# Optimization experiments

Measured on AMD Instinct MI355X. Metric: run time of the kernel, lower is better.

The kernel has to match this reference:

```python
import jax, jax.numpy as jnp
import numpy as np

EMBED_DIM = 768
NUM_HEADS = 12
HEAD_DIM = EMBED_DIM // NUM_HEADS
SCALE = HEAD_DIM ** -0.5
EPS = 1e-5


def _layernorm(x, g, b):
    m = jnp.mean(x, axis=-1, keepdims=True)
    v = jnp.mean(jnp.square(x - m), axis=-1, keepdims=True)
    return (x - m) * jax.lax.rsqrt(v + EPS) * g + b


def setup_inputs() -> dict:
    key = jax.random.key(0)
    ks = jax.random.split(key, 8)
    B, N, D, Hd = 16, 1024, EMBED_DIM, HEAD_DIM
    x = jax.random.normal(ks[0], (B, N, D), dtype=jnp.float32)
    W_qkv = jax.random.normal(ks[1], (D, 3 * D), dtype=jnp.float32) * (D ** -0.5)
    b_qkv = jnp.zeros((3 * D,), dtype=jnp.float32)
    W_proj = jax.random.normal(ks[2], (D, D), dtype=jnp.float32) * (D ** -0.5)
    b_proj = jnp.zeros((D,), dtype=jnp.float32)
    return {
        "x": x,
        "ln_g": jnp.ones((D,), jnp.float32), "ln_b": jnp.zeros((D,), jnp.float32),
        "W_qkv": W_qkv, "b_qkv": b_qkv,
        "qn_g": jnp.ones((Hd,), jnp.float32), "qn_b": jnp.zeros((Hd,), jnp.float32),
        "kn_g": jnp.ones((Hd,), jnp.float32), "kn_b": jnp.zeros((Hd,), jnp.float32),
        "W_proj": W_proj, "b_proj": b_proj,
    }


def reference(x, ln_g, ln_b, W_qkv, b_qkv, qn_g, qn_b, kn_g, kn_b, W_proj, b_proj):
    B, N, D = x.shape
    H, Hd = NUM_HEADS, HEAD_DIM
    xn = _layernorm(x, ln_g, ln_b)                      # qkv_norm (pre-LN of embed_dim)
    qkv = xn @ W_qkv + b_qkv                            # [B,N,3D]
    qkv = qkv.reshape(B, N, 3, H, Hd)
    q = jnp.transpose(qkv[:, :, 0], (0, 2, 1, 3))       # [B,H,N,Hd]
    k = jnp.transpose(qkv[:, :, 1], (0, 2, 1, 3))
    v = jnp.transpose(qkv[:, :, 2], (0, 2, 1, 3))
    q = _layernorm(q, qn_g, qn_b)                       # per-head QK LayerNorm
    k = _layernorm(k, kn_g, kn_b)
    attn = jnp.einsum("bhnd,bhmd->bhnm", q, k) * SCALE
    attn = jax.nn.softmax(attn, axis=-1)
    out = jnp.einsum("bhnm,bhmd->bhnd", attn, v)        # [B,H,N,Hd]
    out = jnp.transpose(out, (0, 2, 1, 3)).reshape(B, N, D)
    return out @ W_proj + b_proj
```

## Files before the change

### kernel.cpp

```cpp
#include <hip/hip_runtime.h>

typedef _Float16 half8 __attribute__((ext_vector_type(8)));
typedef _Float16 half4 __attribute__((ext_vector_type(4)));
typedef float f32x4 __attribute__((ext_vector_type(4)));

#define B_    16
#define N_    1024
#define D_    768
#define H_    12
#define M_    (B_ * N_)
#define QKVN_ 2304
#define EPS_  1e-5f
#define QS_   0.18033688011112042f

__device__ __forceinline__ float exp2_fast(float x) {
#if __has_builtin(__builtin_amdgcn_exp2f)
    return __builtin_amdgcn_exp2f(x);
#else
    return __builtin_exp2f(x);
#endif
}

__device__ __forceinline__ void gl16(const _Float16* g, _Float16* l) {
    __builtin_amdgcn_global_load_lds((const __attribute__((address_space(1))) void*)g,
                                     (__attribute__((address_space(3))) void*)l, 16, 0, 0);
}

__global__ __launch_bounds__(256) void convert_w(const float* __restrict__ Wqkv,
                                                 const float* __restrict__ Wproj,
                                                 _Float16* __restrict__ wqkvT,
                                                 _Float16* __restrict__ wprojT) {
    __shared__ float T[64][65];
    int t = blockIdx.x;
    const float* W; _Float16* O; int NW, k0, n0;
    if (t < 432) { W = Wqkv;  O = wqkvT;  NW = QKVN_; k0 = (t % 12) * 64; n0 = (t / 12) * 64; }
    else { t -= 432; W = Wproj; O = wprojT; NW = D_;  k0 = (t % 12) * 64; n0 = (t / 12) * 64; }
    int c = threadIdx.x & 63, r4 = threadIdx.x >> 6;
#pragma unroll
    for (int i = 0; i < 16; ++i) {
        int r = i * 4 + r4;
        T[r][c] = W[(size_t)(k0 + r) * NW + n0 + c];
    }
    __syncthreads();
#pragma unroll
    for (int i = 0; i < 16; ++i) {
        int r = i * 4 + r4;
        O[(size_t)(n0 + r) * D_ + k0 + c] = (_Float16)T[c][r];
    }
}

__global__ __launch_bounds__(256) void ln_embed(const float* __restrict__ x,
                                                const float* __restrict__ g,
                                                const float* __restrict__ bb,
                                                _Float16* __restrict__ xn) {
    int row = blockIdx.x;
    int tid = threadIdx.x;
    const float* xr = x + (size_t)row * D_;
    float v0 = xr[tid], v1 = xr[tid + 256], v2 = xr[tid + 512];
    float s = v0 + v1 + v2;
    float q = v0 * v0 + v1 * v1 + v2 * v2;
#pragma unroll
    for (int m = 32; m >= 1; m >>= 1) {
        s += __shfl_xor(s, m);
        q += __shfl_xor(q, m);
    }
    __shared__ float ss[4], qq[4];
    int wave = tid >> 6;
    if ((tid & 63) == 0) { ss[wave] = s; qq[wave] = q; }
    __syncthreads();
    float S = ss[0] + ss[1] + ss[2] + ss[3];
    float Q = qq[0] + qq[1] + qq[2] + qq[3];
    float mean = S * (1.f / 768.f);
    float var  = Q * (1.f / 768.f) - mean * mean;
    float rstd = rsqrtf(var + EPS_);
    _Float16* xo = xn + (size_t)row * D_;
    xo[tid]       = (_Float16)((v0 - mean) * rstd * g[tid]       + bb[tid]);
    xo[tid + 256] = (_Float16)((v1 - mean) * rstd * g[tid + 256] + bb[tid + 256]);
    xo[tid + 512] = (_Float16)((v2 - mean) * rstd * g[tid + 512] + bb[tid + 512]);
}

__global__ __launch_bounds__(256) void gemm_qkv(const _Float16* __restrict__ A,
                                                const _Float16* __restrict__ BT,
                                                const float* __restrict__ bias,
                                                const float* __restrict__ qn_g,
                                                const float* __restrict__ qn_b,
                                                const float* __restrict__ kn_g,
                                                const float* __restrict__ kn_b,
                                                _Float16* __restrict__ qo,
                                                _Float16* __restrict__ ko,
                                                _Float16* __restrict__ vt) {
    __shared__ _Float16 As[128 * 32];
    __shared__ _Float16 Bs[128 * 32];
    const int K = D_;
    int bswz = (blockIdx.x & 7) * 288 + (blockIdx.x >> 3);
    int m0 = (bswz % 128) * 128, n0 = (bswz / 128) * 128;
    int tid = threadIdx.x;
    int wave = tid >> 6, lane = tid & 63;
    int wm = wave >> 1, wn = wave & 1;
    int lg = lane >> 4, l15 = lane & 15;
    int xorr = (l15 >> 1) & 3;
    f32x4 acc[4][4] = {};
    for (int k0 = 0; k0 < K; k0 += 32) {
#pragma unroll
        for (int i = 0; i < 2; ++i) {
            int cb = (i * 4 + wave) * 64;
            int chunk = cb + lane;
            int r = chunk >> 2, c = chunk & 3;
            int cg = c ^ ((r >> 1) & 3);
            gl16(&A[(size_t)(m0 + r) * K + k0 + cg * 8], &As[cb * 8]);
            gl16(&BT[(size_t)(n0 + r) * K + k0 + cg * 8], &Bs[cb * 8]);
        }
        __syncthreads();
        half8 af[4], bf[4];
#pragma unroll
        for (int i = 0; i < 4; ++i) {
            af[i] = *(const half8*)&As[(wm * 64 + i * 16 + l15) * 32 + (lg ^ xorr) * 8];
            bf[i] = *(const half8*)&Bs[(wn * 64 + i * 16 + l15) * 32 + (lg ^ xorr) * 8];
        }
#pragma unroll
        for (int mi = 0; mi < 4; ++mi)
#pragma unroll
            for (int ni = 0; ni < 4; ++ni)
                acc[mi][ni] = __builtin_amdgcn_mfma_f32_16x16x32_f16(af[mi], bf[ni], acc[mi][ni], 0, 0, 0);
        __syncthreads();
    }

    int col0 = n0 + wn * 64;
    int s = col0 / 768;
    int hcol = (col0 % 768) >> 6;
    float qkvb[4];
#pragma unroll
    for (int ni = 0; ni < 4; ++ni) qkvb[ni] = bias[col0 + ni * 16 + l15];

    if (s == 2) {
#pragma unroll
        for (int mi = 0; mi < 4; ++mi) {
            int r0 = m0 + wm * 64 + mi * 16 + lg * 4;
            int bidx = r0 >> 10, pos = r0 & 1023;
            int kvblk = pos >> 5, h = (pos >> 4) & 1, lgR = (pos >> 2) & 3;
            size_t vbase = ((size_t)(bidx * H_ + hcol) * 32 + kvblk) * 4;
#pragma unroll
            for (int ni = 0; ni < 4; ++ni) {
                half4 h4;
#pragma unroll
                for (int j = 0; j < 4; ++j) h4[j] = (_Float16)(acc[mi][ni][j] + qkvb[ni]);
                *(half4*)&vt[(vbase + ni) * 512 + lgR * 128 + l15 * 8 + h * 4] = h4;
            }
        }
    } else {
        const float* gg = (s == 0) ? qn_g : kn_g;
        const float* bb = (s == 0) ? qn_b : kn_b;
        float gv[4], bv[4];
#pragma unroll
        for (int ni = 0; ni < 4; ++ni) { gv[ni] = gg[ni * 16 + l15]; bv[ni] = bb[ni * 16 + l15]; }
#pragma unroll
        for (int mi = 0; mi < 4; ++mi) {
#pragma unroll
            for (int j = 0; j < 4; ++j) {
                float v[4];
                float sm = 0.f, sq = 0.f;
#pragma unroll
                for (int ni = 0; ni < 4; ++ni) {
                    v[ni] = acc[mi][ni][j] + qkvb[ni];
                    sm += v[ni];
                    sq += v[ni] * v[ni];
                }
#pragma unroll
                for (int msk = 1; msk < 16; msk <<= 1) {
                    sm += __shfl_xor(sm, msk);
                    sq += __shfl_xor(sq, msk);
                }
                float mean = sm * (1.f / 64.f);
                float var  = sq * (1.f / 64.f) - mean * mean;
                float rstd = rsqrtf(var + EPS_);
                int row = m0 + wm * 64 + mi * 16 + lg * 4 + j;
                int bidx = row >> 10, pos = row & 1023;
                if (s == 0) {
                    size_t rbase = ((size_t)(bidx * H_ + hcol) * 1024 + pos) * 64;
#pragma unroll
                    for (int ni = 0; ni < 4; ++ni) {
                        float o = (v[ni] - mean) * rstd * gv[ni] + bv[ni];
                        qo[rbase + ni * 16 + l15] = (_Float16)(o * QS_);
                    }
                } else {
                    int kvblk = pos >> 5, nh = (pos >> 4) & 1, l15R = pos & 15;
                    size_t base2 = ((size_t)(bidx * H_ + hcol) * 32 + kvblk) * 4 + nh * 2;
#pragma unroll
                    for (int ni = 0; ni < 4; ++ni) {
                        float o = (v[ni] - mean) * rstd * gv[ni] + bv[ni];
                        int ks = ni >> 1, lgR = ((ni & 1) << 1) | (l15 >> 3), elem = l15 & 7;
                        ko[(base2 + ks) * 512 + lgR * 128 + l15R * 8 + elem] = (_Float16)o;
                    }
                }
            }
        }
    }
}

struct KV {
    half8 kf[2][2];
    half8 vf[4];
};

__device__ __forceinline__ void ldKV(KV& s, const _Float16* kp, const _Float16* vp, int kvblk) {
    const _Float16* kb = kp + (size_t)kvblk * 2048;
#pragma unroll
    for (int nh = 0; nh < 2; ++nh)
#pragma unroll
        for (int ks = 0; ks < 2; ++ks)
            s.kf[nh][ks] = *(const half8*)(kb + (nh * 2 + ks) * 512);
    const _Float16* vb = vp + (size_t)kvblk * 2048;
#pragma unroll
    for (int di = 0; di < 4; ++di)
        s.vf[di] = *(const half8*)(vb + di * 512);
}

__device__ __forceinline__ void blockKV(const KV& s, const half8 (&qf)[4][2],
                                        f32x4 (&oacc)[4][4], f32x4 (&lacc)[4],
                                        half8 ones) {
#pragma unroll
    for (int mi = 0; mi < 4; ++mi) {
        f32x4 a0 = {}, a1 = {};
#pragma unroll
        for (int ks = 0; ks < 2; ++ks) {
            a0 = __builtin_amdgcn_mfma_f32_16x16x32_f16(s.kf[0][ks], qf[mi][ks], a0, 0, 0, 0);
            a1 = __builtin_amdgcn_mfma_f32_16x16x32_f16(s.kf[1][ks], qf[mi][ks], a1, 0, 0, 0);
        }
        half8 pf;
#pragma unroll
        for (int j = 0; j < 4; ++j) {
            pf[j]     = (_Float16)exp2_fast(a0[j]);
            pf[j + 4] = (_Float16)exp2_fast(a1[j]);
        }
        lacc[mi] = __builtin_amdgcn_mfma_f32_16x16x32_f16(ones, pf, lacc[mi], 0, 0, 0);
#pragma unroll
        for (int di = 0; di < 4; ++di)
            oacc[mi][di] = __builtin_amdgcn_mfma_f32_16x16x32_f16(s.vf[di], pf, oacc[mi][di], 0, 0, 0);
    }
}

__global__ __launch_bounds__(128, 2) void attn(const _Float16* __restrict__ qg,
                                               const _Float16* __restrict__ kg,
                                               const _Float16* __restrict__ vtg,
                                               _Float16* __restrict__ o) {
    int bphys = blockIdx.x;
    int jj = (bphys & 7) * 192 + (bphys >> 3);
    int bh = jj >> 3, qt = jj & 7;
    int b = bh / H_, h = bh % H_;
    int tid = threadIdx.x;
    int wid = tid >> 6, lane = tid & 63;
    int lg = lane >> 4, l15 = lane & 15;
    size_t base = (size_t)bh << 10;
    int qw0 = qt * 128 + wid * 64;

    const _Float16* qrow = qg + (base + qw0 + l15) * 64 + lg * 8;
    half8 qf[4][2];
#pragma unroll
    for (int mi = 0; mi < 4; ++mi)
#pragma unroll
        for (int ks = 0; ks < 2; ++ks)
            qf[mi][ks] = *(const half8*)(qrow + mi * 1024 + ks * 32);

    const _Float16* kp = kg + (size_t)bh * 65536 + lane * 8;
    const _Float16* vp = vtg + (size_t)bh * 65536 + lane * 8;

    half8 ones;
#pragma unroll
    for (int i = 0; i < 8; ++i) ones[i] = (_Float16)1.0f;

    f32x4 oacc[4][4] = {};
    f32x4 lacc[4] = {};

    KV s0, s1;
    ldKV(s0, kp, vp, 0);
    for (int t = 0; t < 16; ++t) {
        ldKV(s1, kp, vp, (2 * t + 1) & 31);
        blockKV(s0, qf, oacc, lacc, ones);
        ldKV(s0, kp, vp, (2 * t + 2) & 31);
        blockKV(s1, qf, oacc, lacc, ones);
    }

#pragma unroll
    for (int mi = 0; mi < 4; ++mi) {
        float inv = 1.f / lacc[mi][0];
        int q = qw0 + mi * 16 + l15;
        size_t rowb = ((size_t)(b * N_ + q)) * D_ + h * 64 + lg * 4;
#pragma unroll
        for (int di = 0; di < 4; ++di) {
            half4 h4;
#pragma unroll
            for (int j = 0; j < 4; ++j) h4[j] = (_Float16)(oacc[mi][di][j] * inv);
            *(half4*)&o[rowb + di * 16] = h4;
        }
    }
}

__global__ __launch_bounds__(256) void gemm_proj(const _Float16* __restrict__ A,
                                                 const _Float16* __restrict__ BT,
                                                 const float* __restrict__ bias,
                                                 float* __restrict__ out) {
    __shared__ _Float16 As[128 * 32];
    __shared__ _Float16 Bs[128 * 32];
    const int K = D_;
    int bswz = (blockIdx.x & 7) * 96 + (blockIdx.x >> 3);
    int m0 = (bswz % 128) * 128, n0 = (bswz / 128) * 128;
    int tid = threadIdx.x;
    int wave = tid >> 6, lane = tid & 63;
    int wm = wave >> 1, wn = wave & 1;
    int lg = lane >> 4, l15 = lane & 15;
    int xorr = (l15 >> 1) & 3;
    f32x4 acc[4][4] = {};
    for (int k0 = 0; k0 < K; k0 += 32) {
#pragma unroll
        for (int i = 0; i < 2; ++i) {
            int cb = (i * 4 + wave) * 64;
            int chunk = cb + lane;
            int r = chunk >> 2, c = chunk & 3;
            int cg = c ^ ((r >> 1) & 3);
            gl16(&A[(size_t)(m0 + r) * K + k0 + cg * 8], &As[cb * 8]);
            gl16(&BT[(size_t)(n0 + r) * K + k0 + cg * 8], &Bs[cb * 8]);
        }
        __syncthreads();
        half8 af[4], bf[4];
#pragma unroll
        for (int i = 0; i < 4; ++i) {
            af[i] = *(const half8*)&As[(wm * 64 + i * 16 + l15) * 32 + (lg ^ xorr) * 8];
            bf[i] = *(const half8*)&Bs[(wn * 64 + i * 16 + l15) * 32 + (lg ^ xorr) * 8];
        }
#pragma unroll
        for (int mi = 0; mi < 4; ++mi)
#pragma unroll
            for (int ni = 0; ni < 4; ++ni)
                acc[mi][ni] = __builtin_amdgcn_mfma_f32_16x16x32_f16(af[mi], bf[ni], acc[mi][ni], 0, 0, 0);
        __syncthreads();
    }
#pragma unroll
    for (int mi = 0; mi < 4; ++mi)
#pragma unroll
        for (int ni = 0; ni < 4; ++ni) {
            int col = n0 + wn * 64 + ni * 16 + l15;
            float bv = bias[col];
#pragma unroll
            for (int j = 0; j < 4; ++j) {
                int row = m0 + wm * 64 + mi * 16 + lg * 4 + j;
                out[(size_t)row * D_ + col] = acc[mi][ni][j] + bv;
            }
        }
}

extern "C" void kernel_launch(void* const* d_in, const int* in_sizes, int n_in,
                              void* d_out, int out_size, void* d_ws, size_t ws_size,
                              hipStream_t stream) {
    const float* x      = (const float*)d_in[0];
    const float* ln_g   = (const float*)d_in[1];
    const float* ln_b   = (const float*)d_in[2];
    const float* W_qkv  = (const float*)d_in[3];
    const float* b_qkv  = (const float*)d_in[4];
    const float* qn_g   = (const float*)d_in[5];
    const float* qn_b   = (const float*)d_in[6];
    const float* kn_g   = (const float*)d_in[7];
    const float* kn_b   = (const float*)d_in[8];
    const float* W_proj = (const float*)d_in[9];
    const float* b_proj = (const float*)d_in[10];
    float* out = (float*)d_out;
    char* ws = (char*)d_ws;

    constexpr size_t XN_SZ    = (size_t)M_ * D_ * 2;
    constexpr size_t WQKVT_SZ = (size_t)QKVN_ * D_ * 2;
    constexpr size_t WPROJT_SZ= (size_t)D_ * D_ * 2;
    constexpr size_t HEAD_SZ  = (size_t)B_ * H_ * N_ * 64 * 2;

    _Float16* xn     = (_Float16*)(ws);
    _Float16* wqkvT  = (_Float16*)(ws + XN_SZ);
    _Float16* wprojT = (_Float16*)(ws + XN_SZ + WQKVT_SZ);
    _Float16* qb     = (_Float16*)(ws + XN_SZ + WQKVT_SZ + WPROJT_SZ);
    _Float16* kb     = (_Float16*)((char*)qb + HEAD_SZ);
    _Float16* vtb    = (_Float16*)((char*)kb + HEAD_SZ);
    _Float16* ao     = xn;

    convert_w<<<576, 256, 0, stream>>>(W_qkv, W_proj, wqkvT, wprojT);
    ln_embed<<<M_, 256, 0, stream>>>(x, ln_g, ln_b, xn);
    gemm_qkv<<<M_ / 128 * (QKVN_ / 128), 256, 0, stream>>>(xn, wqkvT, b_qkv,
                                                           qn_g, qn_b, kn_g, kn_b,
                                                           qb, kb, vtb);
    attn<<<B_ * H_ * (N_ / 128), 128, 0, stream>>>(qb, kb, vtb, ao);
    gemm_proj<<<M_ / 128 * (D_ / 128), 256, 0, stream>>>(ao, wprojT, b_proj, out);
}
```

Measured before the change: 233.3 us.

## Double-buffer LDS tiles in QKV and proj GEMMs and remap blocks per XCD

Both GEMM kernels now keep two LDS buffers and prefetch the next K-slice with global_load_lds while the current slice feeds the MFMAs. This removes one barrier per iteration and hides global load latency behind compute. The block-to-tile mapping also changes so each XCD owns a contiguous band of M rows and walks across all N tiles, which should improve L2 reuse of the A rows. The cost is double the LDS per block, which may lower occupancy.

```diff
diff --git a/kernel.cpp b/kernel.cpp
--- a/kernel.cpp
+++ b/kernel.cpp
@@ -89,33 +89,41 @@
                                                 _Float16* __restrict__ qo,
                                                 _Float16* __restrict__ ko,
                                                 _Float16* __restrict__ vt) {
-    __shared__ _Float16 As[128 * 32];
-    __shared__ _Float16 Bs[128 * 32];
+    __shared__ _Float16 As[2][128 * 32];
+    __shared__ _Float16 Bs[2][128 * 32];
     const int K = D_;
-    int bswz = (blockIdx.x & 7) * 288 + (blockIdx.x >> 3);
-    int m0 = (bswz % 128) * 128, n0 = (bswz / 128) * 128;
+    int xcd = blockIdx.x & 7, loc = blockIdx.x >> 3;
+    int m0 = (xcd * 16 + loc / 18) * 128;
+    int n0 = (loc % 18) * 128;
     int tid = threadIdx.x;
     int wave = tid >> 6, lane = tid & 63;
     int wm = wave >> 1, wn = wave & 1;
     int lg = lane >> 4, l15 = lane & 15;
     int xorr = (l15 >> 1) & 3;
-    f32x4 acc[4][4] = {};
-    for (int k0 = 0; k0 < K; k0 += 32) {
+
+    auto stage = [&](int b, int k0) {
 #pragma unroll
         for (int i = 0; i < 2; ++i) {
             int cb = (i * 4 + wave) * 64;
             int chunk = cb + lane;
             int r = chunk >> 2, c = chunk & 3;
             int cg = c ^ ((r >> 1) & 3);
-            gl16(&A[(size_t)(m0 + r) * K + k0 + cg * 8], &As[cb * 8]);
-            gl16(&BT[(size_t)(n0 + r) * K + k0 + cg * 8], &Bs[cb * 8]);
-        }
-        __syncthreads();
+            gl16(&A[(size_t)(m0 + r) * K + k0 + cg * 8], &As[b][cb * 8]);
+            gl16(&BT[(size_t)(n0 + r) * K + k0 + cg * 8], &Bs[b][cb * 8]);
+        }
+    };
+
+    f32x4 acc[4][4] = {};
+    stage(0, 0);
+    __syncthreads();
+    for (int t = 0; t < 24; ++t) {
+        int cur = t & 1;
+        if (t < 23) stage(cur ^ 1, (t + 1) * 32);
         half8 af[4], bf[4];
 #pragma unroll
         for (int i = 0; i < 4; ++i) {
-            af[i] = *(const half8*)&As[(wm * 64 + i * 16 + l15) * 32 + (lg ^ xorr) * 8];
-            bf[i] = *(const half8*)&Bs[(wn * 64 + i * 16 + l15) * 32 + (lg ^ xorr) * 8];
+            af[i] = *(const half8*)&As[cur][(wm * 64 + i * 16 + l15) * 32 + (lg ^ xorr) * 8];
+            bf[i] = *(const half8*)&Bs[cur][(wn * 64 + i * 16 + l15) * 32 + (lg ^ xorr) * 8];
         }
 #pragma unroll
         for (int mi = 0; mi < 4; ++mi)
@@ -299,33 +307,41 @@
                                                  const _Float16* __restrict__ BT,
                                                  const float* __restrict__ bias,
                                                  float* __restrict__ out) {
-    __shared__ _Float16 As[128 * 32];
-    __shared__ _Float16 Bs[128 * 32];
+    __shared__ _Float16 As[2][128 * 32];
+    __shared__ _Float16 Bs[2][128 * 32];
     const int K = D_;
-    int bswz = (blockIdx.x & 7) * 96 + (blockIdx.x >> 3);
-    int m0 = (bswz % 128) * 128, n0 = (bswz / 128) * 128;
+    int xcd = blockIdx.x & 7, loc = blockIdx.x >> 3;
+    int m0 = (xcd * 16 + loc / 6) * 128;
+    int n0 = (loc % 6) * 128;
     int tid = threadIdx.x;
     int wave = tid >> 6, lane = tid & 63;
     int wm = wave >> 1, wn = wave & 1;
     int lg = lane >> 4, l15 = lane & 15;
     int xorr = (l15 >> 1) & 3;
-    f32x4 acc[4][4] = {};
-    for (int k0 = 0; k0 < K; k0 += 32) {
+
+    auto stage = [&](int b, int k0) {
 #pragma unroll
         for (int i = 0; i < 2; ++i) {
             int cb = (i * 4 + wave) * 64;
             int chunk = cb + lane;
             int r = chunk >> 2, c = chunk & 3;
             int cg = c ^ ((r >> 1) & 3);
-            gl16(&A[(size_t)(m0 + r) * K + k0 + cg * 8], &As[cb * 8]);
-            gl16(&BT[(size_t)(n0 + r) * K + k0 + cg * 8], &Bs[cb * 8]);
-        }
-        __syncthreads();
+            gl16(&A[(size_t)(m0 + r) * K + k0 + cg * 8], &As[b][cb * 8]);
+            gl16(&BT[(size_t)(n0 + r) * K + k0 + cg * 8], &Bs[b][cb * 8]);
+        }
+    };
+
+    f32x4 acc[4][4] = {};
+    stage(0, 0);
+    __syncthreads();
+    for (int t = 0; t < 24; ++t) {
+        int cur = t & 1;
+        if (t < 23) stage(cur ^ 1, (t + 1) * 32);
         half8 af[4], bf[4];
 #pragma unroll
         for (int i = 0; i < 4; ++i) {
-            af[i] = *(const half8*)&As[(wm * 64 + i * 16 + l15) * 32 + (lg ^ xorr) * 8];
-            bf[i] = *(const half8*)&Bs[(wn * 64 + i * 16 + l15) * 32 + (lg ^ xorr) * 8];
+            af[i] = *(const half8*)&As[cur][(wm * 64 + i * 16 + l15) * 32 + (lg ^ xorr) * 8];
+            bf[i] = *(const half8*)&Bs[cur][(wn * 64 + i * 16 + l15) * 32 + (lg ^ xorr) * 8];
         }
 #pragma unroll
         for (int mi = 0; mi < 4; ++mi)
```

New measurement: 226.3 us. -3.0%, faster.
